# Kernel tuning notes

Hardware: AMD Instinct MI355X
Metric: run time of the kernel (lower is better)

Reference implementation:

```python
import jax, jax.numpy as jnp
import numpy as np

ALPHA = 0.2          # LeakyReLU negative slope
NEG_FILL = -9e15     # mask value used by the original module


def setup_inputs() -> dict:
    key = jax.random.key(0)
    k1, k2, k3, k4 = jax.random.split(key, 4)
    N, D, H, F = 4096, 512, 8, 64  # nhid*nheads == embedding_dim
    h = jax.random.normal(k1, (N, D), dtype=jnp.float32)
    adj = jax.random.randint(k2, (N, N), 0, 2, dtype=jnp.int32)
    # per-head linear projection weights (no bias) and attention vectors
    W = jax.random.normal(k3, (H, D, F), dtype=jnp.float32) * (1.0 / np.sqrt(D))
    a = jax.random.normal(k4, (H, 2 * F), dtype=jnp.float32) * 0.1
    return {"h": h, "adj": adj, "W": W, "a": a}


def reference(h, adj, W, a):
    H, D, F = W.shape
    N = h.shape[0]
    # per-head projection: [H, N, F]
    hp = jnp.einsum('nd,hdf->hnf', h, W)
    # score(i,j) = leakyrelu(a[:F].h_i + a[F:].h_j)  (decomposed broadcast-add,
    # same math as the original N*N concat construction)
    a_src, a_dst = a[:, :F], a[:, F:]
    f_src = jnp.einsum('hnf,hf->hn', hp, a_src)  # [H, N]
    f_dst = jnp.einsum('hnf,hf->hn', hp, a_dst)  # [H, N]
    e = jax.nn.leaky_relu(f_src[:, :, None] + f_dst[:, None, :], ALPHA)  # [H,N,N]
    e = jnp.where(adj[None] > 0, e, NEG_FILL)
    att = jax.nn.softmax(e, axis=-1)  # softmax over neighbors j (dim=1 in torch)
    out = jnp.einsum('hij,hjf->hif', att, hp)  # [H, N, F]
    # concat heads -> [N, H*F], then ELU
    out = jnp.transpose(out, (1, 0, 2)).reshape(N, H * F)
    return jax.nn.elu(out)
```

## Files before the change

kernel.cpp:

```cpp
#include <hip/hip_runtime.h>

#define NN 4096
#define DD 512
#define HH 8
#define FF 64
#define LRELU_ALPHA 0.2f
#define SP 72

typedef __attribute__((ext_vector_type(8))) short bf16x8;
typedef __attribute__((ext_vector_type(4))) float f32x4;

__device__ __forceinline__ float f4c(const float4& v, int k) {
    return k == 0 ? v.x : (k == 1 ? v.y : (k == 2 ? v.z : v.w));
}
__device__ __forceinline__ void f4s(float4& v, int k, float x) {
    if (k == 0) v.x = x; else if (k == 1) v.y = x; else if (k == 2) v.z = x; else v.w = x;
}
__device__ __forceinline__ unsigned short f2bf(float x) {
    unsigned u = __float_as_uint(x);
    return (unsigned short)((u + 0x7fffu + ((u >> 16) & 1u)) >> 16);
}
__device__ __forceinline__ float bf2f(unsigned short h) {
    return __uint_as_float(((unsigned)h) << 16);
}
__device__ __forceinline__ unsigned fkey(float x) {
    unsigned u = __float_as_uint(x);
    return (u & 0x80000000u) ? ~u : (u | 0x80000000u);
}
__device__ __forceinline__ float funkey(unsigned k) {
    unsigned u = (k & 0x80000000u) ? (k ^ 0x80000000u) : ~k;
    return __uint_as_float(u);
}
__device__ __forceinline__ void sync_lds() {
    asm volatile("s_waitcnt lgkmcnt(0)\n\ts_barrier" ::: "memory");
}

__global__ __launch_bounds__(256) void k_prep(const int* __restrict__ adj,
                                              const float* __restrict__ W,
                                              unsigned* __restrict__ adjw,
                                              unsigned short* __restrict__ wt_hi,
                                              unsigned short* __restrict__ wt_lo,
                                              unsigned* __restrict__ mxkey,
                                              float* __restrict__ hpsum) {
    __shared__ float tile[64][65];
    int b = blockIdx.x, t = threadIdx.x;
    if (b < 4096) {
        int lane = t & 63;
        #pragma unroll
        for (int i = 0; i < 16; i++) {
            int tid = ((b * 16 + i) << 8) + t;
            unsigned long long mask = __ballot(adj[tid] > 0);
            if (lane == 0) {
                int base = tid >> 5;
                adjw[base] = (unsigned)mask;
                adjw[base + 1] = (unsigned)(mask >> 32);
            }
        }
    } else if (b < 4160) {
        int idx = b - 4096;
        int h = idx >> 3;
        int d0 = (idx & 7) * 64;
        #pragma unroll
        for (int kidx = 0; kidx < 4; kidx++) {
            int id = t + 256 * kidx;
            int dd = id >> 4, f4i = (id & 15) * 4;
            float4 v = *(const float4*)(W + ((size_t)(h * DD + d0 + dd)) * FF + f4i);
            tile[dd][f4i] = v.x; tile[dd][f4i + 1] = v.y;
            tile[dd][f4i + 2] = v.z; tile[dd][f4i + 3] = v.w;
        }
        __syncthreads();
        int f = t >> 2, c = (t & 3) * 16;
        union { unsigned short s[16]; uint4 v[2]; } hb, lb;
        #pragma unroll
        for (int q = 0; q < 16; q++) {
            float v = tile[c + q][f];
            unsigned short hi = f2bf(v);
            hb.s[q] = hi;
            lb.s[q] = f2bf(v - bf2f(hi));
        }
        uint4* dh = (uint4*)(wt_hi + ((size_t)h * FF + f) * DD + d0 + c);
        uint4* dl = (uint4*)(wt_lo + ((size_t)h * FF + f) * DD + d0 + c);
        dh[0] = hb.v[0]; dh[1] = hb.v[1];
        dl[0] = lb.v[0]; dl[1] = lb.v[1];
    } else {
        if (t < 16) mxkey[t] = 0u;
        hpsum[t] = 0.f;
        hpsum[t + 256] = 0.f;
    }
}

__global__ __launch_bounds__(256) void k_hp_mfma(const float* __restrict__ hmat,
                                                 const unsigned short* __restrict__ whi,
                                                 const unsigned short* __restrict__ wlo,
                                                 const float* __restrict__ a,
                                                 unsigned short* __restrict__ hpT_hi,
                                                 float* __restrict__ fs,
                                                 float* __restrict__ fd,
                                                 float* __restrict__ hpsum,
                                                 unsigned* __restrict__ mxkey) {
    __shared__ char smem[4 * 64 * SP * 2];
    unsigned short* ah = (unsigned short*)smem;
    unsigned short* al = ah + 64 * SP;
    unsigned short* bh = al + 64 * SP;
    unsigned short* bl = bh + 64 * SP;

    int t = threadIdx.x;
    int h = blockIdx.y;
    int n0 = blockIdx.x * 64;
    int lane = t & 63;
    int w = t >> 6;
    int R0 = (w >> 1) * 32, F0 = (w & 1) * 32;
    int am = lane & 15, aq = lane >> 4;
    int sr = t >> 2, sc = (t & 3) * 16;

    const float* gha = hmat + (size_t)(n0 + sr) * DD;
    const unsigned short* gbh = whi + ((size_t)h * FF + sr) * DD;
    const unsigned short* gbl = wlo + ((size_t)h * FF + sr) * DD;

    float4 p0, p1, p2, p3;
    uint4 w0, w1, x0, x1;
    auto gload = [&](int kk) {
        p0 = *(const float4*)(gha + kk + sc);
        p1 = *(const float4*)(gha + kk + sc + 4);
        p2 = *(const float4*)(gha + kk + sc + 8);
        p3 = *(const float4*)(gha + kk + sc + 12);
        const uint4* s2 = (const uint4*)(gbh + kk + sc);
        const uint4* s3 = (const uint4*)(gbl + kk + sc);
        w0 = s2[0]; w1 = s2[1]; x0 = s3[0]; x1 = s3[1];
    };
    auto wstage = [&]() {
        union { unsigned short s[16]; uint4 v[2]; } hb, lb;
        #pragma unroll
        for (int q = 0; q < 16; q++) {
            float v = q < 4 ? f4c(p0, q) : q < 8 ? f4c(p1, q - 4)
                      : q < 12 ? f4c(p2, q - 8) : f4c(p3, q - 12);
            unsigned short hi = f2bf(v);
            hb.s[q] = hi;
            lb.s[q] = f2bf(v - bf2f(hi));
        }
        *(uint4*)(ah + sr * SP + sc) = hb.v[0]; *(uint4*)(ah + sr * SP + sc + 8) = hb.v[1];
        *(uint4*)(al + sr * SP + sc) = lb.v[0]; *(uint4*)(al + sr * SP + sc + 8) = lb.v[1];
        *(uint4*)(bh + sr * SP + sc) = w0; *(uint4*)(bh + sr * SP + sc + 8) = w1;
        *(uint4*)(bl + sr * SP + sc) = x0; *(uint4*)(bl + sr * SP + sc + 8) = x1;
    };

    f32x4 acc[2][2] = {};
    gload(0);
    for (int kk = 0; kk < DD; kk += 64) {
        wstage();
        if (kk + 64 < DD) gload(kk + 64);
        sync_lds();
        #pragma unroll
        for (int k2 = 0; k2 < 2; k2++) {
            int ko = k2 * 32 + aq * 8;
            bf16x8 a0h = *(const bf16x8*)(ah + (R0 + am) * SP + ko);
            bf16x8 a1h = *(const bf16x8*)(ah + (R0 + 16 + am) * SP + ko);
            bf16x8 a0l = *(const bf16x8*)(al + (R0 + am) * SP + ko);
            bf16x8 a1l = *(const bf16x8*)(al + (R0 + 16 + am) * SP + ko);
            bf16x8 b0h = *(const bf16x8*)(bh + (F0 + am) * SP + ko);
            bf16x8 b1h = *(const bf16x8*)(bh + (F0 + 16 + am) * SP + ko);
            bf16x8 b0l = *(const bf16x8*)(bl + (F0 + am) * SP + ko);
            bf16x8 b1l = *(const bf16x8*)(bl + (F0 + 16 + am) * SP + ko);
            acc[0][0] = __builtin_amdgcn_mfma_f32_16x16x32_bf16(a0h, b0h, acc[0][0], 0, 0, 0);
            acc[0][1] = __builtin_amdgcn_mfma_f32_16x16x32_bf16(a0h, b1h, acc[0][1], 0, 0, 0);
            acc[1][0] = __builtin_amdgcn_mfma_f32_16x16x32_bf16(a1h, b0h, acc[1][0], 0, 0, 0);
            acc[1][1] = __builtin_amdgcn_mfma_f32_16x16x32_bf16(a1h, b1h, acc[1][1], 0, 0, 0);
            acc[0][0] = __builtin_amdgcn_mfma_f32_16x16x32_bf16(a0h, b0l, acc[0][0], 0, 0, 0);
            acc[0][1] = __builtin_amdgcn_mfma_f32_16x16x32_bf16(a0h, b1l, acc[0][1], 0, 0, 0);
            acc[1][0] = __builtin_amdgcn_mfma_f32_16x16x32_bf16(a1h, b0l, acc[1][0], 0, 0, 0);
            acc[1][1] = __builtin_amdgcn_mfma_f32_16x16x32_bf16(a1h, b1l, acc[1][1], 0, 0, 0);
            acc[0][0] = __builtin_amdgcn_mfma_f32_16x16x32_bf16(a0l, b0h, acc[0][0], 0, 0, 0);
            acc[0][1] = __builtin_amdgcn_mfma_f32_16x16x32_bf16(a0l, b1h, acc[0][1], 0, 0, 0);
            acc[1][0] = __builtin_amdgcn_mfma_f32_16x16x32_bf16(a1l, b0h, acc[1][0], 0, 0, 0);
            acc[1][1] = __builtin_amdgcn_mfma_f32_16x16x32_bf16(a1l, b1h, acc[1][1], 0, 0, 0);
        }
        sync_lds();
    }

    unsigned* tt = (unsigned*)smem;
    float* rs = (float*)(smem + 17408);
    float* rd = rs + 256;
    float* ash = rd + 256;
    if (t < 128) ash[t] = a[h * 2 * FF + t];
    int col = lane & 15, rbase = (lane >> 4) * 4;
    #pragma unroll
    for (int m16 = 0; m16 < 2; m16++) {
        #pragma unroll
        for (int n16 = 0; n16 < 2; n16++) {
            #pragma unroll
            for (int r = 0; r < 4; r++) {
                int nl = R0 + m16 * 16 + rbase + r;
                int f = F0 + n16 * 16 + col;
                float v = acc[m16][n16][r];
                unsigned short hi = f2bf(v);
                unsigned short lo = f2bf(v - bf2f(hi));
                tt[f * 68 + nl] = (unsigned)hi | ((unsigned)lo << 16);
            }
        }
    }
    __syncthreads();
    {
        int f = t >> 2, c = (t & 3) * 16;
        union { unsigned short s[16]; uint4 v[2]; } hb;
        float csum = 0.f;
        #pragma unroll
        for (int q = 0; q < 16; q++) {
            unsigned u = tt[f * 68 + c + q];
            hb.s[q] = (unsigned short)(u & 0xffffu);
            csum += bf2f((unsigned short)(u & 0xffffu)) + bf2f((unsigned short)(u >> 16));
        }
        uint4* dh = (uint4*)(hpT_hi + ((size_t)h * FF + f) * NN + n0 + c);
        dh[0] = hb.v[0]; dh[1] = hb.v[1];
        csum += __shfl_xor(csum, 1);
        csum += __shfl_xor(csum, 2);
        if ((t & 3) == 0) unsafeAtomicAdd(hpsum + h * FF + f, csum);
    }
    {
        int n = t & 63, g = t >> 6;
        float fsp = 0.f, fdp = 0.f;
        #pragma unroll
        for (int q = 0; q < 16; q++) {
            int f = g * 16 + q;
            unsigned u = tt[f * 68 + n];
            float v = bf2f((unsigned short)(u & 0xffffu)) + bf2f((unsigned short)(u >> 16));
            fsp += v * ash[f];
            fdp += v * ash[64 + f];
        }
        rs[g * 64 + n] = fsp;
        rd[g * 64 + n] = fdp;
    }
    __syncthreads();
    if (t < 64) {
        float fdv = rd[t] + rd[64 + t] + rd[128 + t] + rd[192 + t];
        fs[(size_t)h * NN + n0 + t] = rs[t] + rs[64 + t] + rs[128 + t] + rs[192 + t];
        fd[(size_t)h * NN + n0 + t] = fdv;
        unsigned key = fkey(fdv);
        #pragma unroll
        for (int off = 32; off; off >>= 1) key = max(key, (unsigned)__shfl_xor((int)key, off));
        if (t == 0) atomicMax(mxkey + h, key);
    }
}

__global__ __launch_bounds__(256) void k_attn(const float* __restrict__ fs,
                                              const float* __restrict__ fd,
                                              const unsigned* __restrict__ mxkey,
                                              const unsigned* __restrict__ adjw,
                                              const unsigned short* __restrict__ hpT_hi,
                                              const float* __restrict__ hpsum,
                                              float* __restrict__ outp) {
    __shared__ unsigned short pa[2][32 * SP];
    __shared__ unsigned short hbh[2][64 * SP];
    __shared__ float fss[32], ms[32];

    int t = threadIdx.x;
    int h = blockIdx.y;
    int i0 = blockIdx.x * 32;
    int lane = t & 63;
    int w = t >> 6;

    const float LOG2E = 1.44269504f;
    float mfd = funkey(mxkey[h]);
    if (t < 32) {
        float fsv = fs[(size_t)h * NN + i0 + t];
        fss[t] = fsv;
        float s = fsv + mfd;
        float m = fmaxf(s, LRELU_ALPHA * s);
        ms[t] = m * LOG2E;
    }
    __syncthreads();

    int wr = t >> 3;
    int wc = (t & 7) * 8;
    int sr = t >> 2, sc = (t & 3) * 16;
    int R0 = (w >> 1) * 16, F0 = (w & 1) * 32;
    int am = lane & 15, aq = lane >> 4;
    f32x4 acc[2] = {};
    f32x4 accl = {};
    bf16x8 bones;
    #pragma unroll
    for (int i = 0; i < 8; i++) bones[i] = (short)0x3f80;

    const unsigned short* gH = hpT_hi + (size_t)h * FF * NN;
    const float* fdh = fd + (size_t)h * NN;
    float fsr = fss[wr], mr = ms[wr];

    uint4 rH0, rH1;
    float4 rF0, rF1;
    unsigned rA;
    auto gload = [&](int j0) {
        const uint4* sh = (const uint4*)(gH + (size_t)sr * NN + j0 + sc);
        rH0 = sh[0]; rH1 = sh[1];
        rF0 = *(const float4*)(fdh + j0 + wc);
        rF1 = *(const float4*)(fdh + j0 + wc + 4);
        rA  = adjw[(size_t)(i0 + wr) * (NN / 32) + ((j0 + wc) >> 5)];
    };
    auto wstage = [&](int buf) {
        *(uint4*)(&hbh[buf][sr * SP + sc]) = rH0;
        *(uint4*)(&hbh[buf][sr * SP + sc + 8]) = rH1;
        unsigned bits = rA >> (wc & 31);
        union { unsigned u[4]; uint4 v; } wb;
        #pragma unroll
        for (int q = 0; q < 2; q++) {
            float4 fdv = q ? rF1 : rF0;
            unsigned eu[4];
            #pragma unroll
            for (int b = 0; b < 4; b++) {
                float s = fsr + f4c(fdv, b);
                float l = fmaxf(s, LRELU_ALPHA * s);
                float e = __builtin_amdgcn_exp2f(__builtin_fmaf(l, LOG2E, -mr));
                e = ((bits >> (q * 4 + b)) & 1u) ? e : 0.f;
                eu[b] = __float_as_uint(e);
            }
            wb.u[q * 2]     = __builtin_amdgcn_perm(eu[1], eu[0], 0x07060302);
            wb.u[q * 2 + 1] = __builtin_amdgcn_perm(eu[3], eu[2], 0x07060302);
        }
        *(uint4*)(&pa[buf][wr * SP + wc]) = wb.v;
    };

    gload(0);
    wstage(0);
    gload(64);
    sync_lds();
    for (int k = 0; k < NN / 64; k++) {
        int cur = k & 1;
        #pragma unroll
        for (int k2 = 0; k2 < 2; k2++) {
            int ko = k2 * 32 + aq * 8;
            bf16x8 a0 = *(const bf16x8*)(&pa[cur][(R0 + am) * SP + ko]);
            bf16x8 b0 = *(const bf16x8*)(&hbh[cur][(F0 + am) * SP + ko]);
            bf16x8 b1 = *(const bf16x8*)(&hbh[cur][(F0 + 16 + am) * SP + ko]);
            acc[0] = __builtin_amdgcn_mfma_f32_16x16x32_bf16(a0, b0, acc[0], 0, 0, 0);
            acc[1] = __builtin_amdgcn_mfma_f32_16x16x32_bf16(a0, b1, acc[1], 0, 0, 0);
            accl   = __builtin_amdgcn_mfma_f32_16x16x32_bf16(a0, bones, accl, 0, 0, 0);
        }
        if (k < NN / 64 - 1) {
            wstage(cur ^ 1);
            if (k < NN / 64 - 2) gload((k + 2) * 64);
        }
        sync_lds();
    }

    const float invN = 1.0f / NN;
    int col = lane & 15, rbase = (lane >> 4) * 4;
    #pragma unroll
    for (int r = 0; r < 4; r++) {
        int row = i0 + R0 + rbase + r;
        float l = accl[r];
        float rl = 1.f / l;
        #pragma unroll
        for (int n16 = 0; n16 < 2; n16++) {
            int f = F0 + n16 * 16 + col;
            float v;
            if (l > 0.f) v = acc[n16][r] * rl;
            else         v = hpsum[h * FF + f] * invN;
            v = v > 0.f ? v : __expf(v) - 1.f;
            outp[(size_t)row * (HH * FF) + h * FF + f] = v;
        }
    }
}

extern "C" void kernel_launch(void* const* d_in, const int* in_sizes, int n_in,
                              void* d_out, int out_size, void* d_ws, size_t ws_size,
                              hipStream_t stream) {
    const float* hmat = (const float*)d_in[0];
    const int*   adj  = (const int*)d_in[1];
    const float* W    = (const float*)d_in[2];
    const float* a    = (const float*)d_in[3];
    float* out = (float*)d_out;

    char* ws = (char*)d_ws;
    unsigned short* hpT_hi = (unsigned short*)(ws);
    unsigned*       adjw   = (unsigned*)(ws + (4u << 20));
    unsigned short* wt_hi  = (unsigned short*)(ws + (6u << 20));
    unsigned short* wt_lo  = (unsigned short*)(ws + (6u << 20) + (512u << 10));
    float* fs    = (float*)(ws + (7u << 20));
    float* fd    = (float*)(ws + (7u << 20) + (128u << 10));
    unsigned* mxkey = (unsigned*)(ws + (7u << 20) + (256u << 10));
    float* hpsum = (float*)(mxkey + 16);

    k_prep   <<<dim3(4161),          256, 0, stream>>>(adj, W, adjw, wt_hi, wt_lo,
                                                       mxkey, hpsum);
    k_hp_mfma<<<dim3(64, 8),         256, 0, stream>>>(hmat, wt_hi, wt_lo, a,
                                                       hpT_hi, fs, fd, hpsum, mxkey);
    k_attn   <<<dim3(NN / 32, HH),   256, 0, stream>>>(fs, fd, mxkey, adjw,
                                                       hpT_hi, hpsum, out);
}
```

Measured before the change: 190.0 us.

## Compute attention weights in registers per wave and drop LDS staging

The attention kernel no longer stages the probability tile and hp slices through shared memory. Each wave now owns 16 query rows across all 64 features. It builds the bf16 A fragment directly in registers from fd and the adjacency bits, and loads B fragments straight from global memory with double-buffered register prefetch. The LeakyReLU-exp is rewritten as the max of two precomputed affine terms, and the block covers 64 rows. This removes LDS traffic and block-wide barriers, but each wave now reloads hp from global or L2 with no sharing between waves, which raises cache bandwidth demand. It also halves the grid size.

```diff
diff --git a/kernel.cpp b/kernel.cpp
--- a/kernel.cpp
+++ b/kernel.cpp
@@ -248,110 +248,102 @@
                                               const unsigned short* __restrict__ hpT_hi,
                                               const float* __restrict__ hpsum,
                                               float* __restrict__ outp) {
-    __shared__ unsigned short pa[2][32 * SP];
-    __shared__ unsigned short hbh[2][64 * SP];
-    __shared__ float fss[32], ms[32];
-
     int t = threadIdx.x;
     int h = blockIdx.y;
-    int i0 = blockIdx.x * 32;
+    int wv = t >> 6;
+    int q0 = blockIdx.x * 64 + wv * 16;
     int lane = t & 63;
-    int w = t >> 6;
+    int am = lane & 15, aq = lane >> 4;
 
     const float LOG2E = 1.44269504f;
     float mfd = funkey(mxkey[h]);
-    if (t < 32) {
-        float fsv = fs[(size_t)h * NN + i0 + t];
-        fss[t] = fsv;
-        float s = fsv + mfd;
-        float m = fmaxf(s, LRELU_ALPHA * s);
-        ms[t] = m * LOG2E;
-    }
-    __syncthreads();
-
-    int wr = t >> 3;
-    int wc = (t & 7) * 8;
-    int sr = t >> 2, sc = (t & 3) * 16;
-    int R0 = (w >> 1) * 16, F0 = (w & 1) * 32;
-    int am = lane & 15, aq = lane >> 4;
-    f32x4 acc[2] = {};
+    float fsr = fs[(size_t)h * NN + q0 + am];
+    float sM = fsr + mfd;
+    float mr = fmaxf(sM, LRELU_ALPHA * sM) * LOG2E;
+    float Ac = __builtin_fmaf(fsr, LOG2E, -mr);
+    float Bc = __builtin_fmaf(fsr, LRELU_ALPHA * LOG2E, -mr);
+
+    const unsigned short* pB = hpT_hi + ((size_t)h * FF + am) * NN + aq * 8;
+    const float* pfd = fd + (size_t)h * NN + aq * 8;
+    const unsigned* prow = adjw + (size_t)(q0 + am) * (NN / 32);
+    int bsh = aq * 8;
+
+    f32x4 acc[4] = {};
     f32x4 accl = {};
     bf16x8 bones;
     #pragma unroll
     for (int i = 0; i < 8; i++) bones[i] = (short)0x3f80;
 
-    const unsigned short* gH = hpT_hi + (size_t)h * FF * NN;
-    const float* fdh = fd + (size_t)h * NN;
-    float fsr = fss[wr], mr = ms[wr];
-
-    uint4 rH0, rH1;
-    float4 rF0, rF1;
-    unsigned rA;
-    auto gload = [&](int j0) {
-        const uint4* sh = (const uint4*)(gH + (size_t)sr * NN + j0 + sc);
-        rH0 = sh[0]; rH1 = sh[1];
-        rF0 = *(const float4*)(fdh + j0 + wc);
-        rF1 = *(const float4*)(fdh + j0 + wc + 4);
-        rA  = adjw[(size_t)(i0 + wr) * (NN / 32) + ((j0 + wc) >> 5)];
-    };
-    auto wstage = [&](int buf) {
-        *(uint4*)(&hbh[buf][sr * SP + sc]) = rH0;
-        *(uint4*)(&hbh[buf][sr * SP + sc + 8]) = rH1;
-        unsigned bits = rA >> (wc & 31);
-        union { unsigned u[4]; uint4 v; } wb;
+    bf16x8 Xb0, Xb1, Xb2, Xb3; float4 Xf0, Xf1; unsigned Xw;
+    bf16x8 Yb0, Yb1, Yb2, Yb3; float4 Yf0, Yf1; unsigned Yw;
+
+    auto gloadX = [&](int j0) {
+        Xb0 = *(const bf16x8*)(pB + j0);
+        Xb1 = *(const bf16x8*)(pB + (size_t)16 * NN + j0);
+        Xb2 = *(const bf16x8*)(pB + (size_t)32 * NN + j0);
+        Xb3 = *(const bf16x8*)(pB + (size_t)48 * NN + j0);
+        Xf0 = *(const float4*)(pfd + j0);
+        Xf1 = *(const float4*)(pfd + j0 + 4);
+        Xw  = prow[j0 >> 5];
+    };
+    auto gloadY = [&](int j0) {
+        Yb0 = *(const bf16x8*)(pB + j0);
+        Yb1 = *(const bf16x8*)(pB + (size_t)16 * NN + j0);
+        Yb2 = *(const bf16x8*)(pB + (size_t)32 * NN + j0);
+        Yb3 = *(const bf16x8*)(pB + (size_t)48 * NN + j0);
+        Yf0 = *(const float4*)(pfd + j0);
+        Yf1 = *(const float4*)(pfd + j0 + 4);
+        Yw  = prow[j0 >> 5];
+    };
+    auto compute = [&](bf16x8 b0, bf16x8 b1, bf16x8 b2, bf16x8 b3,
+                       float4 f0, float4 f1, unsigned word) {
+        unsigned bits = word >> bsh;
+        unsigned eu[8];
         #pragma unroll
         for (int q = 0; q < 2; q++) {
-            float4 fdv = q ? rF1 : rF0;
-            unsigned eu[4];
+            float4 fdv = q ? f1 : f0;
             #pragma unroll
             for (int b = 0; b < 4; b++) {
-                float s = fsr + f4c(fdv, b);
-                float l = fmaxf(s, LRELU_ALPHA * s);
-                float e = __builtin_amdgcn_exp2f(__builtin_fmaf(l, LOG2E, -mr));
+                float fdL = f4c(fdv, b) * LOG2E;
+                float t1 = Ac + fdL;
+                float t2 = __builtin_fmaf(fdL, LRELU_ALPHA, Bc);
+                float e = __builtin_amdgcn_exp2f(fmaxf(t1, t2));
                 e = ((bits >> (q * 4 + b)) & 1u) ? e : 0.f;
-                eu[b] = __float_as_uint(e);
+                eu[q * 4 + b] = __float_as_uint(e);
             }
-            wb.u[q * 2]     = __builtin_amdgcn_perm(eu[1], eu[0], 0x07060302);
-            wb.u[q * 2 + 1] = __builtin_amdgcn_perm(eu[3], eu[2], 0x07060302);
-        }
-        *(uint4*)(&pa[buf][wr * SP + wc]) = wb.v;
-    };
-
-    gload(0);
-    wstage(0);
-    gload(64);
-    sync_lds();
-    for (int k = 0; k < NN / 64; k++) {
-        int cur = k & 1;
-        #pragma unroll
-        for (int k2 = 0; k2 < 2; k2++) {
-            int ko = k2 * 32 + aq * 8;
-            bf16x8 a0 = *(const bf16x8*)(&pa[cur][(R0 + am) * SP + ko]);
-            bf16x8 b0 = *(const bf16x8*)(&hbh[cur][(F0 + am) * SP + ko]);
-            bf16x8 b1 = *(const bf16x8*)(&hbh[cur][(F0 + 16 + am) * SP + ko]);
-            acc[0] = __builtin_amdgcn_mfma_f32_16x16x32_bf16(a0, b0, acc[0], 0, 0, 0);
-            acc[1] = __builtin_amdgcn_mfma_f32_16x16x32_bf16(a0, b1, acc[1], 0, 0, 0);
-            accl   = __builtin_amdgcn_mfma_f32_16x16x32_bf16(a0, bones, accl, 0, 0, 0);
-        }
-        if (k < NN / 64 - 1) {
-            wstage(cur ^ 1);
-            if (k < NN / 64 - 2) gload((k + 2) * 64);
-        }
-        sync_lds();
+        }
+        union { unsigned u[4]; bf16x8 v; } af;
+        af.u[0] = __builtin_amdgcn_perm(eu[1], eu[0], 0x07060302);
+        af.u[1] = __builtin_amdgcn_perm(eu[3], eu[2], 0x07060302);
+        af.u[2] = __builtin_amdgcn_perm(eu[5], eu[4], 0x07060302);
+        af.u[3] = __builtin_amdgcn_perm(eu[7], eu[6], 0x07060302);
+        acc[0] = __builtin_amdgcn_mfma_f32_16x16x32_bf16(af.v, b0, acc[0], 0, 0, 0);
+        acc[1] = __builtin_amdgcn_mfma_f32_16x16x32_bf16(af.v, b1, acc[1], 0, 0, 0);
+        acc[2] = __builtin_amdgcn_mfma_f32_16x16x32_bf16(af.v, b2, acc[2], 0, 0, 0);
+        acc[3] = __builtin_amdgcn_mfma_f32_16x16x32_bf16(af.v, b3, acc[3], 0, 0, 0);
+        accl   = __builtin_amdgcn_mfma_f32_16x16x32_bf16(af.v, bones, accl, 0, 0, 0);
+    };
+
+    gloadX(0);
+    for (int j0 = 0; j0 < NN; j0 += 64) {
+        gloadY(j0 + 32);
+        compute(Xb0, Xb1, Xb2, Xb3, Xf0, Xf1, Xw);
+        if (j0 + 64 < NN) gloadX(j0 + 64);
+        compute(Yb0, Yb1, Yb2, Yb3, Yf0, Yf1, Yw);
     }
 
     const float invN = 1.0f / NN;
     int col = lane & 15, rbase = (lane >> 4) * 4;
     #pragma unroll
     for (int r = 0; r < 4; r++) {
-        int row = i0 + R0 + rbase + r;
+        int row = q0 + rbase + r;
         float l = accl[r];
         float rl = 1.f / l;
         #pragma unroll
-        for (int n16 = 0; n16 < 2; n16++) {
-            int f = F0 + n16 * 16 + col;
+        for (int Fi = 0; Fi < 4; Fi++) {
+            int f = Fi * 16 + col;
             float v;
-            if (l > 0.f) v = acc[n16][r] * rl;
+            if (l > 0.f) v = acc[Fi][r] * rl;
             else         v = hpsum[h * FF + f] * invN;
             v = v > 0.f ? v : __expf(v) - 1.f;
             outp[(size_t)row * (HH * FF) + h * FF + f] = v;
@@ -382,6 +374,6 @@
                                                        mxkey, hpsum);
     k_hp_mfma<<<dim3(64, 8),         256, 0, stream>>>(hmat, wt_hi, wt_lo, a,
                                                        hpT_hi, fs, fd, hpsum, mxkey);
-    k_attn   <<<dim3(NN / 32, HH),   256, 0, stream>>>(fs, fd, mxkey, adjw,
+    k_attn   <<<dim3(NN / 64, HH),   256, 0, stream>>>(fs, fd, mxkey, adjw,
                                                        hpT_hi, hpsum, out);
 }
```

After: 286.7 us. 1.51x slower.
